# Optimization experiments

Measured on AMD Instinct MI355X. Metric: run time of the kernel, lower is better.

The kernel has to match this reference:

```python
import jax, jax.numpy as jnp
import numpy as np

K = 5            # kernel_size for gaussian and bilateral
PAD = K // 2
SIGMA = 1.0          # gaussian sigma / bilateral sigma_spatial
SIGMA_INT = 0.1      # bilateral sigma_intensity


def _spatial_kernel():
    coords = jnp.arange(K, dtype=jnp.float32) - K // 2
    x, y = jnp.meshgrid(coords, coords, indexing='ij')
    return jnp.exp(-(x ** 2 + y ** 2) / (2.0 * SIGMA ** 2))  # (K, K), unnormalized


def setup_inputs() -> dict:
    key = jax.random.key(0)
    images = jax.random.uniform(key, (8, 3, 512, 512), dtype=jnp.float32)
    return {"images": images}


def _gaussian_filter(images):
    g = _spatial_kernel()
    g = g / g.sum()
    kernel = jnp.tile(g[None, None], (3, 1, 1, 1))  # (3,1,K,K) depthwise
    return jax.lax.conv_general_dilated(
        images, kernel, window_strides=(1, 1),
        padding=[(PAD, PAD), (PAD, PAD)],
        dimension_numbers=('NCHW', 'OIHW', 'NCHW'),
        feature_group_count=3)


def _bilateral_filter(images):
    B, C, H, W = images.shape
    padded = jnp.pad(images, ((0, 0), (0, 0), (PAD, PAD), (PAD, PAD)), mode='reflect')
    # im2col: (B, C, K*K, H, W) -- fixed 25-iteration loop over kernel offsets
    patches = jnp.stack([padded[:, :, i:i + H, j:j + W]
                         for i in range(K) for j in range(K)], axis=2)
    center = patches[:, :, K * K // 2:K * K // 2 + 1]  # (B,C,1,H,W)
    iw = jnp.exp(-(patches - center) ** 2 / (2.0 * SIGMA_INT ** 2))
    sw = _spatial_kernel().reshape(1, 1, K * K, 1, 1)
    w = sw * iw
    w = w / (w.sum(axis=2, keepdims=True) + 1e-8)
    return (patches * w).sum(axis=2)  # (B,C,H,W)


def reference(images):
    # AdaptiveAntiAlias.forward(images, mode='auto')
    gaussian_out = _gaussian_filter(images)
    bilateral_out = _bilateral_filter(images)
    return 0.6 * gaussian_out + 0.4 * bilateral_out
```

## Files before the change

kernel.cpp:

```cpp
#include <hip/hip_runtime.h>

#define IMG_H 512
#define IMG_W 512
#define HW    (IMG_H * IMG_W)
#define NCH   24

__device__ __forceinline__ float fexp2(float x) {
#if __has_builtin(__builtin_amdgcn_exp2f)
    return __builtin_amdgcn_exp2f(x);
#else
    float r; asm("v_exp_f32 %0, %1" : "=v"(r) : "v"(x)); return r;
#endif
}
__device__ __forceinline__ float frcp(float x) {
#if __has_builtin(__builtin_amdgcn_rcpf)
    return __builtin_amdgcn_rcpf(x);
#else
    float r; asm("v_rcp_f32 %0, %1" : "=v"(r) : "v"(x)); return r;
#endif
}

__device__ __forceinline__ constexpr double exs(int r2) {
    return (r2 == 0) ? 1.0
         : (r2 == 1) ? 0.60653065971263342
         : (r2 == 2) ? 0.36787944117144233
         : (r2 == 4) ? 0.13533528323661270
         : (r2 == 5) ? 0.08208499862389880
         : (r2 == 8) ? 0.01831563888873418 : 0.0;
}
#define SSUM 6.16892408102888092
__device__ __forceinline__ constexpr float k1(int d)  { return (float)exs(d * d); }
__device__ __forceinline__ constexpr float k1n(int d) { return (float)(exs(d * d) / SSUM); }
#define NEG50  -72.134752044448169f
#define LG     -0.72134752044448169f

#define PER_CH_B (4 * 128 + 508 * 2)
#define N_B (PER_CH_B * NCH)
#define XG_INT 126
#define YT_INT 254
#define PER_CH_T (XG_INT * YT_INT)
#define N_INT (PER_CH_T * NCH)
#define N_TOTAL (N_B + N_INT)

#define BLK 64

__global__ __launch_bounds__(BLK) void aa_kernel(const float* __restrict__ in,
                                                 float* __restrict__ out) {
    const int gid = blockIdx.x * BLK + threadIdx.x;

    if (gid < N_B) {
        const int ch = gid / PER_CH_B;
        const int r  = gid - ch * PER_CH_B;
        int y, x0;
        if (r < 512) {
            const int q = r >> 7;
            y  = (q < 2) ? q : q + 508;
            x0 = (r & 127) << 2;
        } else {
            const int t = r - 512;
            y  = 2 + (t >> 1);
            x0 = (t & 1) ? (IMG_W - 4) : 0;
        }
        const float* __restrict__ img = in + ch * HW;

        int ry[5]; float krow[5];
        #pragma unroll
        for (int i = 0; i < 5; ++i) {
            const int yy = y + i - 2;
            const int ryy = (yy < 0) ? -yy : ((yy >= IMG_H) ? 2 * IMG_H - 2 - yy : yy);
            ry[i] = ryy * IMG_W;
            krow[i] = ((yy >= 0) & (yy < IMG_H)) ? k1(i - 2) : 0.0f;
        }
        int rx[8]; float xin[8];
        #pragma unroll
        for (int c = 0; c < 8; ++c) {
            const int xx = x0 + c - 2;
            rx[c] = (xx < 0) ? -xx : ((xx >= IMG_W) ? 2 * IMG_W - 2 - xx : xx);
            xin[c] = ((xx >= 0) & (xx < IMG_W)) ? 1.0f : 0.0f;
        }
        float v[5][8];
        #pragma unroll
        for (int i = 0; i < 5; ++i) {
            #pragma unroll
            for (int c = 0; c < 8; ++c) v[i][c] = img[ry[i] + rx[c]];
        }

        float csm[8];
        #pragma unroll
        for (int c = 0; c < 8; ++c) {
            float s = krow[0] * v[0][c];
            s = fmaf(krow[1], v[1][c], s);
            s = fmaf(krow[2], v[2][c], s);
            s = fmaf(krow[3], v[3][c], s);
            s = fmaf(krow[4], v[4][c], s);
            csm[c] = s * xin[c];
        }

        float res[4];
        #pragma unroll
        for (int p = 0; p < 4; ++p) {
            const float ctr = v[2][2 + p];
            float arg[24];
            {
                int t = 0;
                #pragma unroll
                for (int i = 0; i < 5; ++i) {
                    #pragma unroll
                    for (int j = 0; j < 5; ++j) {
                        if (i == 2 && j == 2) continue;
                        const int r2 = (i - 2) * (i - 2) + (j - 2) * (j - 2);
                        const float d = v[i][p + j] - ctr;
                        arg[t] = fmaf(d * d, NEG50, LG * (float)r2);
                        ++t;
                    }
                }
            }
            float w[24];
            #pragma unroll
            for (int k = 0; k < 24; ++k) w[k] = fexp2(arg[k]);

            float ws0 = 1.0f, ws1 = 0.f, ws2 = 0.f, ws3 = 0.f;
            float bs0 = ctr,  bs1 = 0.f, bs2 = 0.f, bs3 = 0.f;
            {
                int t = 0;
                #pragma unroll
                for (int i = 0; i < 5; ++i) {
                    #pragma unroll
                    for (int j = 0; j < 5; ++j) {
                        if (i == 2 && j == 2) continue;
                        const float vv = v[i][p + j];
                        if ((t & 3) == 0)      { ws0 += w[t]; bs0 = fmaf(w[t], vv, bs0); }
                        else if ((t & 3) == 1) { ws1 += w[t]; bs1 = fmaf(w[t], vv, bs1); }
                        else if ((t & 3) == 2) { ws2 += w[t]; bs2 = fmaf(w[t], vv, bs2); }
                        else                   { ws3 += w[t]; bs3 = fmaf(w[t], vv, bs3); }
                        ++t;
                    }
                }
            }
            const float wsum = (ws0 + ws1) + (ws2 + ws3);
            const float bsum = (bs0 + bs1) + (bs2 + bs3);

            float g = k1n(2) * csm[p];
            g = fmaf(k1n(1), csm[p + 1], g);
            g = fmaf(k1n(0), csm[p + 2], g);
            g = fmaf(k1n(1), csm[p + 3], g);
            g = fmaf(k1n(2), csm[p + 4], g);

            res[p] = fmaf(0.6f, g, 0.4f * (bsum * frcp(wsum + 1e-8f)));
        }

        float4* o4 = (float4*)(out + ch * HW + y * IMG_W + x0);
        *o4 = make_float4(res[0], res[1], res[2], res[3]);
    } else {
        const int ig = gid - N_B;
        if (ig >= N_INT) return;
        const int ch  = ig / PER_CH_T;
        const int rem = ig - ch * PER_CH_T;
        const int ty  = rem / XG_INT;
        const int y0  = 2 + ty * 2;
        const int x0  = 4 + (rem - ty * XG_INT) * 4;

        const float* __restrict__ img = in + ch * HW;
        const float* base = img + (y0 - 2) * IMG_W + (x0 - 2);

        float2 L[6][4];
        #pragma unroll
        for (int r = 0; r < 6; ++r) {
            const float2* rp = (const float2*)(base + r * IMG_W);
            #pragma unroll
            for (int c = 0; c < 4; ++c) L[r][c] = rp[c];
        }
        #define V(r, c) (((c) & 1) ? L[r][(c) >> 1].y : L[r][(c) >> 1].x)

        float cs[2][8];
        #pragma unroll
        for (int yr = 0; yr < 2; ++yr) {
            #pragma unroll
            for (int c = 0; c < 8; ++c) {
                float s = k1(2) * V(yr + 0, c);
                s = fmaf(k1(1), V(yr + 1, c), s);
                s = fmaf(k1(0), V(yr + 2, c), s);
                s = fmaf(k1(1), V(yr + 3, c), s);
                s = fmaf(k1(2), V(yr + 4, c), s);
                cs[yr][c] = s;
            }
        }

        float res[2][4];
        #pragma unroll
        for (int yr = 0; yr < 2; ++yr) {
            #pragma unroll
            for (int p = 0; p < 4; ++p) {
                const float ctr = V(2 + yr, 2 + p);

                float arg[24];
                {
                    int t = 0;
                    #pragma unroll
                    for (int i = 0; i < 5; ++i) {
                        #pragma unroll
                        for (int j = 0; j < 5; ++j) {
                            if (i == 2 && j == 2) continue;
                            const int r2 = (i - 2) * (i - 2) + (j - 2) * (j - 2);
                            const float d = V(yr + i, p + j) - ctr;
                            arg[t] = fmaf(d * d, NEG50, LG * (float)r2);
                            ++t;
                        }
                    }
                }
                float w[24];
                #pragma unroll
                for (int k = 0; k < 24; ++k) w[k] = fexp2(arg[k]);

                float ws0 = 1.0f, ws1 = 0.f, ws2 = 0.f, ws3 = 0.f;
                float bs0 = ctr,  bs1 = 0.f, bs2 = 0.f, bs3 = 0.f;
                {
                    int t = 0;
                    #pragma unroll
                    for (int i = 0; i < 5; ++i) {
                        #pragma unroll
                        for (int j = 0; j < 5; ++j) {
                            if (i == 2 && j == 2) continue;
                            const float vv = V(yr + i, p + j);
                            if ((t & 3) == 0)      { ws0 += w[t]; bs0 = fmaf(w[t], vv, bs0); }
                            else if ((t & 3) == 1) { ws1 += w[t]; bs1 = fmaf(w[t], vv, bs1); }
                            else if ((t & 3) == 2) { ws2 += w[t]; bs2 = fmaf(w[t], vv, bs2); }
                            else                   { ws3 += w[t]; bs3 = fmaf(w[t], vv, bs3); }
                            ++t;
                        }
                    }
                }
                const float wsum = (ws0 + ws1) + (ws2 + ws3);
                const float bsum = (bs0 + bs1) + (bs2 + bs3);

                float g = k1n(2) * cs[yr][p];
                g = fmaf(k1n(1), cs[yr][p + 1], g);
                g = fmaf(k1n(0), cs[yr][p + 2], g);
                g = fmaf(k1n(1), cs[yr][p + 3], g);
                g = fmaf(k1n(2), cs[yr][p + 4], g);

                res[yr][p] = fmaf(0.6f, g, 0.4f * (bsum * frcp(wsum + 1e-8f)));
            }
        }
        #undef V

        float* op = out + ch * HW + y0 * IMG_W + x0;
        *(float4*)op           = make_float4(res[0][0], res[0][1], res[0][2], res[0][3]);
        *(float4*)(op + IMG_W) = make_float4(res[1][0], res[1][1], res[1][2], res[1][3]);
    }
}

extern "C" void kernel_launch(void* const* d_in, const int* in_sizes, int n_in,
                              void* d_out, int out_size, void* d_ws, size_t ws_size,
                              hipStream_t stream) {
    const float* img = (const float*)d_in[0];
    float* out = (float*)d_out;
    const int blocks = (N_TOTAL + BLK - 1) / BLK;
    aa_kernel<<<blocks, BLK, 0, stream>>>(img, out);
}
```

Measured before the change: 39.20 us.

## Share symmetric bilateral weights across 4x4 pixel tile per thread

Each interior thread now handles a 4x4 output tile instead of 2x4 and exploits the symmetry of the intensity weight (w(p,q)=w(q,p)), so each exp2 between two pixels inside the tile is computed once and added to both. This cuts transcendental and arithmetic work per output, and the larger tile also amortizes the loaded halo. Block size is raised from 64 to 256. The cost is higher register pressure (8x8 inputs plus 16 accumulators), which may reduce occupancy.

New measurement: 38.95 us. About the same (-0.6%).

```diff
diff --git a/kernel.cpp b/kernel.cpp
--- a/kernel.cpp
+++ b/kernel.cpp
@@ -36,17 +36,17 @@
 
 #define PER_CH_B (4 * 128 + 508 * 2)
 #define N_B (PER_CH_B * NCH)
-#define XG_INT 126
-#define YT_INT 254
-#define PER_CH_T (XG_INT * YT_INT)
+#define XT 126
+#define YT 127
+#define PER_CH_T (XT * YT)
 #define N_INT (PER_CH_T * NCH)
 #define N_TOTAL (N_B + N_INT)
 
-#define BLK 64
-
-__global__ __launch_bounds__(BLK) void aa_kernel(const float* __restrict__ in,
+__device__ __constant__ const int c_unused = 0;
+
+__global__ __launch_bounds__(256) void aa_kernel(const float* __restrict__ in,
                                                  float* __restrict__ out) {
-    const int gid = blockIdx.x * BLK + threadIdx.x;
+    const int gid = blockIdx.x * 256 + threadIdx.x;
 
     if (gid < N_B) {
         const int ch = gid / PER_CH_B;
@@ -156,97 +156,120 @@
         if (ig >= N_INT) return;
         const int ch  = ig / PER_CH_T;
         const int rem = ig - ch * PER_CH_T;
-        const int ty  = rem / XG_INT;
-        const int y0  = 2 + ty * 2;
-        const int x0  = 4 + (rem - ty * XG_INT) * 4;
+        const int ty  = rem / XT;
+        const int y0  = 2 + ty * 4;
+        const int x0  = 4 + (rem - ty * XT) * 4;
 
         const float* __restrict__ img = in + ch * HW;
         const float* base = img + (y0 - 2) * IMG_W + (x0 - 2);
 
-        float2 L[6][4];
-        #pragma unroll
-        for (int r = 0; r < 6; ++r) {
+        float v[8][8];
+        #pragma unroll
+        for (int r = 0; r < 8; ++r) {
             const float2* rp = (const float2*)(base + r * IMG_W);
             #pragma unroll
-            for (int c = 0; c < 4; ++c) L[r][c] = rp[c];
-        }
-        #define V(r, c) (((c) & 1) ? L[r][(c) >> 1].y : L[r][(c) >> 1].x)
-
-        float cs[2][8];
-        #pragma unroll
-        for (int yr = 0; yr < 2; ++yr) {
+            for (int c = 0; c < 4; ++c) {
+                const float2 t = rp[c];
+                v[r][2 * c]     = t.x;
+                v[r][2 * c + 1] = t.y;
+            }
+        }
+
+        float ws[16], bs[16];
+        #pragma unroll
+        for (int p = 0; p < 16; ++p) {
+            const int pr = p >> 2, pc = p & 3;
+            ws[p] = 1.0f;
+            bs[p] = v[pr + 2][pc + 2];
+        }
+
+        constexpr int PDI[12] = {0, 0, 1,  1, 1, 1, 1, 2,  2, 2, 2, 2};
+        constexpr int PDJ[12] = {1, 2, -2, -1, 0, 1, 2, -2, -1, 0, 1, 2};
+
+        #pragma unroll
+        for (int o = 0; o < 12; ++o) {
+            const int di = PDI[o], dj = PDJ[o];
+            const int r2 = di * di + dj * dj;
+            const float lsw = LG * (float)r2;
+            float wt[16];
+            #pragma unroll
+            for (int p = 0; p < 16; ++p) {
+                const int pr = p >> 2, pc = p & 3;
+                const float d = v[pr + 2 + di][pc + 2 + dj] - v[pr + 2][pc + 2];
+                wt[p] = fexp2(fmaf(d * d, NEG50, lsw));
+            }
+            #pragma unroll
+            for (int p = 0; p < 16; ++p) {
+                const int pr = p >> 2, pc = p & 3;
+                const float vp = v[pr + 2][pc + 2];
+                const float vt = v[pr + 2 + di][pc + 2 + dj];
+                ws[p] += wt[p];
+                bs[p] = fmaf(wt[p], vt, bs[p]);
+                const int qr = pr + di, qc = pc + dj;
+                if (qr >= 0 && qr < 4 && qc >= 0 && qc < 4) {
+                    const int q = qr * 4 + qc;
+                    ws[q] += wt[p];
+                    bs[q] = fmaf(wt[p], vp, bs[q]);
+                }
+            }
+        }
+        #pragma unroll
+        for (int o = 0; o < 12; ++o) {
+            const int di = -PDI[o], dj = -PDJ[o];
+            const int r2 = di * di + dj * dj;
+            const float lsw = LG * (float)r2;
+            float wt[16];
+            #pragma unroll
+            for (int p = 0; p < 16; ++p) {
+                const int pr = p >> 2, pc = p & 3;
+                const int qr = pr + di, qc = pc + dj;
+                if (qr < 0 || qr >= 4 || qc < 0 || qc >= 4) {
+                    const float d = v[pr + 2 + di][pc + 2 + dj] - v[pr + 2][pc + 2];
+                    wt[p] = fexp2(fmaf(d * d, NEG50, lsw));
+                }
+            }
+            #pragma unroll
+            for (int p = 0; p < 16; ++p) {
+                const int pr = p >> 2, pc = p & 3;
+                const int qr = pr + di, qc = pc + dj;
+                if (qr < 0 || qr >= 4 || qc < 0 || qc >= 4) {
+                    const float vt = v[pr + 2 + di][pc + 2 + dj];
+                    ws[p] += wt[p];
+                    bs[p] = fmaf(wt[p], vt, bs[p]);
+                }
+            }
+        }
+
+        float cs[4][8];
+        #pragma unroll
+        for (int yr = 0; yr < 4; ++yr) {
             #pragma unroll
             for (int c = 0; c < 8; ++c) {
-                float s = k1(2) * V(yr + 0, c);
-                s = fmaf(k1(1), V(yr + 1, c), s);
-                s = fmaf(k1(0), V(yr + 2, c), s);
-                s = fmaf(k1(1), V(yr + 3, c), s);
-                s = fmaf(k1(2), V(yr + 4, c), s);
+                float s = k1(2) * v[yr][c];
+                s = fmaf(k1(1), v[yr + 1][c], s);
+                s = fmaf(k1(0), v[yr + 2][c], s);
+                s = fmaf(k1(1), v[yr + 3][c], s);
+                s = fmaf(k1(2), v[yr + 4][c], s);
                 cs[yr][c] = s;
             }
         }
 
-        float res[2][4];
-        #pragma unroll
-        for (int yr = 0; yr < 2; ++yr) {
-            #pragma unroll
-            for (int p = 0; p < 4; ++p) {
-                const float ctr = V(2 + yr, 2 + p);
-
-                float arg[24];
-                {
-                    int t = 0;
-                    #pragma unroll
-                    for (int i = 0; i < 5; ++i) {
-                        #pragma unroll
-                        for (int j = 0; j < 5; ++j) {
-                            if (i == 2 && j == 2) continue;
-                            const int r2 = (i - 2) * (i - 2) + (j - 2) * (j - 2);
-                            const float d = V(yr + i, p + j) - ctr;
-                            arg[t] = fmaf(d * d, NEG50, LG * (float)r2);
-                            ++t;
-                        }
-                    }
-                }
-                float w[24];
-                #pragma unroll
-                for (int k = 0; k < 24; ++k) w[k] = fexp2(arg[k]);
-
-                float ws0 = 1.0f, ws1 = 0.f, ws2 = 0.f, ws3 = 0.f;
-                float bs0 = ctr,  bs1 = 0.f, bs2 = 0.f, bs3 = 0.f;
-                {
-                    int t = 0;
-                    #pragma unroll
-                    for (int i = 0; i < 5; ++i) {
-                        #pragma unroll
-                        for (int j = 0; j < 5; ++j) {
-                            if (i == 2 && j == 2) continue;
-                            const float vv = V(yr + i, p + j);
-                            if ((t & 3) == 0)      { ws0 += w[t]; bs0 = fmaf(w[t], vv, bs0); }
-                            else if ((t & 3) == 1) { ws1 += w[t]; bs1 = fmaf(w[t], vv, bs1); }
-                            else if ((t & 3) == 2) { ws2 += w[t]; bs2 = fmaf(w[t], vv, bs2); }
-                            else                   { ws3 += w[t]; bs3 = fmaf(w[t], vv, bs3); }
-                            ++t;
-                        }
-                    }
-                }
-                const float wsum = (ws0 + ws1) + (ws2 + ws3);
-                const float bsum = (bs0 + bs1) + (bs2 + bs3);
-
-                float g = k1n(2) * cs[yr][p];
-                g = fmaf(k1n(1), cs[yr][p + 1], g);
-                g = fmaf(k1n(0), cs[yr][p + 2], g);
-                g = fmaf(k1n(1), cs[yr][p + 3], g);
-                g = fmaf(k1n(2), cs[yr][p + 4], g);
-
-                res[yr][p] = fmaf(0.6f, g, 0.4f * (bsum * frcp(wsum + 1e-8f)));
-            }
-        }
-        #undef V
-
         float* op = out + ch * HW + y0 * IMG_W + x0;
-        *(float4*)op           = make_float4(res[0][0], res[0][1], res[0][2], res[0][3]);
-        *(float4*)(op + IMG_W) = make_float4(res[1][0], res[1][1], res[1][2], res[1][3]);
+        #pragma unroll
+        for (int yr = 0; yr < 4; ++yr) {
+            float res[4];
+            #pragma unroll
+            for (int pc = 0; pc < 4; ++pc) {
+                float g = k1n(2) * cs[yr][pc];
+                g = fmaf(k1n(1), cs[yr][pc + 1], g);
+                g = fmaf(k1n(0), cs[yr][pc + 2], g);
+                g = fmaf(k1n(1), cs[yr][pc + 3], g);
+                g = fmaf(k1n(2), cs[yr][pc + 4], g);
+                const int p = yr * 4 + pc;
+                res[pc] = fmaf(0.6f, g, 0.4f * (bs[p] * frcp(ws[p] + 1e-8f)));
+            }
+            *(float4*)(op + yr * IMG_W) = make_float4(res[0], res[1], res[2], res[3]);
+        }
     }
 }
 
@@ -255,6 +278,6 @@
                               hipStream_t stream) {
     const float* img = (const float*)d_in[0];
     float* out = (float*)d_out;
-    const int blocks = (N_TOTAL + BLK - 1) / BLK;
-    aa_kernel<<<blocks, BLK, 0, stream>>>(img, out);
-}
+    const int blocks = (N_TOTAL + 255) / 256;
+    aa_kernel<<<blocks, 256, 0, stream>>>(img, out);
+}
```
